# Kernel tuning notes

Measured on AMD Instinct MI355X. Metric: run time of the kernel, lower is better.

## Reference

```python
import jax, jax.numpy as jnp
import numpy as np

N, M, D, H, T = 8192, 8192, 64, 32, 8
KERNEL_SCALE = 1.0


def setup_inputs() -> dict:
    key = jax.random.key(0)
    ks = jax.random.split(key, 8)
    s1 = 1.0 / np.sqrt(D)
    s2 = 1.0 / np.sqrt(H)
    return {
        "X": jax.random.normal(ks[0], (N, D), jnp.float32),
        "Y": jax.random.normal(ks[1], (M, D), jnp.float32),
        "Y_target": jax.random.normal(ks[2], (M, T), jnp.float32),
        "W1": jax.random.normal(ks[3], (D, H), jnp.float32) * s1,
        "b1": jnp.zeros((H,), jnp.float32),
        "W2": jax.random.normal(ks[4], (H, H), jnp.float32) * s2,
        "b2": jnp.zeros((H,), jnp.float32),
        "W3": jax.random.normal(ks[5], (H, H), jnp.float32) * s2,
        "b3": jnp.zeros((H,), jnp.float32),
    }


def _mlp(x, W1, b1, W2, b2, W3, b3):
    h = jax.nn.relu(x @ W1 + b1)
    h = jax.nn.relu(h @ W2 + b2)
    return jax.nn.relu(h @ W3 + b3)


def reference(X, Y, Y_target, W1, b1, W2, b2, W3, b3):
    Xf = _mlp(X, W1, b1, W2, b2, W3, b3)  # [N, H]
    Yf = _mlp(Y, W1, b1, W2, b2, W3, b3)  # [M, H]
    sq = (
        jnp.sum(Xf * Xf, axis=1, keepdims=True)
        + jnp.sum(Yf * Yf, axis=1)[None, :]
        - 2.0 * (Xf @ Yf.T)
    )
    sq = jnp.maximum(sq, 0.0)  # guard tiny negatives from cancellation
    kernel = jnp.exp(-sq / (2.0 * KERNEL_SCALE**2))  # [N, M]
    weights = kernel / jnp.sum(kernel, axis=1, keepdims=True)
    return weights @ Y_target  # [N, T]
```

## Files before the change

kernel.cpp:

```cpp
#include <hip/hip_runtime.h>
#include <hip/hip_bf16.h>
#include <cstddef>

#define N_ROWS 8192
#define M_ROWS 8192
#define D_IN   64
#define H_DIM  32
#define T_OUT  8

#define NSPLIT   16
#define JSLICE   (M_ROWS / NSPLIT)
#define JTILE    32
#define NTILES   (JSLICE / JTILE)
#define NSTAGES  (NTILES / 2)
#define LOG2E    1.4426950408889634f
#define NHALF_SC (-0.72134752044448169f)

#define YI_OFF  8192
#define CK_OFF  16384
#define STAGEBUF 16640

typedef _Float16 half8  __attribute__((ext_vector_type(8)));
typedef _Float16 half4v __attribute__((ext_vector_type(4)));
typedef __fp16   fp16x2 __attribute__((ext_vector_type(2)));
typedef float    f32x16 __attribute__((ext_vector_type(16)));

__device__ __forceinline__ half8 ld_h8(const _Float16* p) {
    return *(const half8*)p;
}


__global__ __launch_bounds__(256) void prep_kernel(
    const float* __restrict__ X, const float* __restrict__ Y,
    const float* __restrict__ Yt,
    const float* __restrict__ W1, const float* __restrict__ b1,
    const float* __restrict__ W2, const float* __restrict__ b2,
    const float* __restrict__ W3, const float* __restrict__ b3,
    _Float16* __restrict__ fh, _Float16* __restrict__ fl,
    _Float16* __restrict__ yfi, float* __restrict__ ns)
{
    __shared__ float xs [32 * 65];
    __shared__ float w1l[64 * 36];
    __shared__ float w2l[32 * 36];
    __shared__ float w3l[32 * 36];
    __shared__ float h1t[32 * 33];
    __shared__ float h2t[32 * 33];
    __shared__ float psums[8 * 32];
    __shared__ float bl[96];

    const int tid = threadIdx.x;

    if (blockIdx.x >= 512) {
        const int idx = (blockIdx.x - 512) * 256 + tid;
        const int lane = idx & 63;
        const int jtg  = idx >> 6;
        const int g    = jtg & 3;
        const int jt   = jtg >> 2;
        const int t    = lane & 31;
        const int h    = lane >> 5;
        const int j    = jt * 32 + g * 8 + h * 4;
        union { _Float16 hh[8]; uint4 u; } V;
        #pragma unroll
        for (int i = 0; i < 4; ++i) {
            float v = (t < T_OUT) ? Yt[(size_t)(j + i) * T_OUT + t]
                                  : (t == 8 ? 1.0f : 0.0f);
            _Float16 hi = (_Float16)v;
            V.hh[i]     = hi;
            V.hh[4 + i] = (_Float16)(v - (float)hi);
        }
        *(uint4*)(yfi + (size_t)idx * 8) = V.u;
        return;
    }

    const int rowbase = blockIdx.x * 32;
    const bool isX = rowbase < N_ROWS;
    const float* src = isX ? (X + (size_t)rowbase * D_IN)
                           : (Y + (size_t)(rowbase - N_ROWS) * D_IN);

    {
        const float4* g4 = (const float4*)src;
        int i0 = tid * 2;
        float4 v0 = g4[i0], v1 = g4[i0 + 1];
        int f0 = tid * 8;
        int r = f0 >> 6, c = f0 & 63;
        float* dst = xs + r * 65 + c;
        dst[0] = v0.x; dst[1] = v0.y; dst[2] = v0.z; dst[3] = v0.w;
        dst[4] = v1.x; dst[5] = v1.y; dst[6] = v1.z; dst[7] = v1.w;
    }
    {
        const float4* g4 = (const float4*)W1;
        int i0 = tid * 2;
        float4 v0 = g4[i0], v1 = g4[i0 + 1];
        int f0 = tid * 8;
        int r = f0 >> 5, c = f0 & 31;
        float* dst = w1l + r * 36 + c;
        ((float4*)dst)[0] = v0; ((float4*)dst)[1] = v1;
    }
    {
        int f0 = tid * 4;
        int r = f0 >> 5, c = f0 & 31;
        *(float4*)(w2l + r * 36 + c) = ((const float4*)W2)[tid];
        *(float4*)(w3l + r * 36 + c) = ((const float4*)W3)[tid];
    }
    if (tid < 32) { bl[tid] = b1[tid]; bl[32 + tid] = b2[tid]; bl[64 + tid] = b3[tid]; }
    __syncthreads();

    const int r  = tid & 31;
    const int c0 = (tid >> 5) * 4;

    float4 a1 = *(const float4*)(bl + c0);
    #pragma unroll
    for (int k = 0; k < 64; ++k) {
        float xv = xs[r * 65 + k];
        float4 w = *(const float4*)(w1l + k * 36 + c0);
        a1.x = fmaf(xv, w.x, a1.x);
        a1.y = fmaf(xv, w.y, a1.y);
        a1.z = fmaf(xv, w.z, a1.z);
        a1.w = fmaf(xv, w.w, a1.w);
    }
    h1t[(c0 + 0) * 33 + r] = fmaxf(a1.x, 0.f);
    h1t[(c0 + 1) * 33 + r] = fmaxf(a1.y, 0.f);
    h1t[(c0 + 2) * 33 + r] = fmaxf(a1.z, 0.f);
    h1t[(c0 + 3) * 33 + r] = fmaxf(a1.w, 0.f);
    __syncthreads();

    float4 a2 = *(const float4*)(bl + 32 + c0);
    #pragma unroll
    for (int k = 0; k < 32; ++k) {
        float xv = h1t[k * 33 + r];
        float4 w = *(const float4*)(w2l + k * 36 + c0);
        a2.x = fmaf(xv, w.x, a2.x);
        a2.y = fmaf(xv, w.y, a2.y);
        a2.z = fmaf(xv, w.z, a2.z);
        a2.w = fmaf(xv, w.w, a2.w);
    }
    h2t[(c0 + 0) * 33 + r] = fmaxf(a2.x, 0.f);
    h2t[(c0 + 1) * 33 + r] = fmaxf(a2.y, 0.f);
    h2t[(c0 + 2) * 33 + r] = fmaxf(a2.z, 0.f);
    h2t[(c0 + 3) * 33 + r] = fmaxf(a2.w, 0.f);
    __syncthreads();

    float4 a3 = *(const float4*)(bl + 64 + c0);
    #pragma unroll
    for (int k = 0; k < 32; ++k) {
        float xv = h2t[k * 33 + r];
        float4 w = *(const float4*)(w3l + k * 36 + c0);
        a3.x = fmaf(xv, w.x, a3.x);
        a3.y = fmaf(xv, w.y, a3.y);
        a3.z = fmaf(xv, w.z, a3.z);
        a3.w = fmaf(xv, w.w, a3.w);
    }
    float v0 = fmaxf(a3.x, 0.f), v1 = fmaxf(a3.y, 0.f);
    float v2 = fmaxf(a3.z, 0.f), v3 = fmaxf(a3.w, 0.f);

    psums[(tid >> 5) * 32 + r] = v0 * v0 + v1 * v1 + v2 * v2 + v3 * v3;

    const float scale = isX ? LOG2E : 1.0f;
    union { _Float16 h[4]; uint2 u; } hh, ll;
    float sv0 = v0 * scale, sv1 = v1 * scale, sv2 = v2 * scale, sv3 = v3 * scale;
    hh.h[0] = (_Float16)sv0; hh.h[1] = (_Float16)sv1;
    hh.h[2] = (_Float16)sv2; hh.h[3] = (_Float16)sv3;
    ll.h[0] = (_Float16)(sv0 - (float)hh.h[0]);
    ll.h[1] = (_Float16)(sv1 - (float)hh.h[1]);
    ll.h[2] = (_Float16)(sv2 - (float)hh.h[2]);
    ll.h[3] = (_Float16)(sv3 - (float)hh.h[3]);
    {
        const int tile = blockIdx.x;
        const int ch = c0 >> 4, hb = (c0 >> 3) & 1, off = c0 & 7;
        const size_t fi = (((size_t)(tile * 2 + ch) * 64) + hb * 32 + r) * 8 + off;
        *(uint2*)(fh + fi) = hh.u;
        *(uint2*)(fl + fi) = ll.u;
    }

    __syncthreads();
    if (tid < 32) {
        float nrm = 0.f;
        #pragma unroll
        for (int g = 0; g < 8; ++g) nrm += psums[g * 32 + tid];
        ns[rowbase + tid] = NHALF_SC * nrm;
    }
}

__global__ __launch_bounds__(256, 4) void pair_kernel(
    const _Float16* __restrict__ fh, const _Float16* __restrict__ fl,
    const _Float16* __restrict__ yfi, const float* __restrict__ ns,
    float* __restrict__ pout, float* __restrict__ psum)
{
    __shared__ char smem[2 * STAGEBUF];

    const int tid  = threadIdx.x;
    const int wave = tid >> 6;
    const int lane = tid & 63;
    const int n    = lane & 31;
    const int h    = lane >> 5;

    const int rowtile = blockIdx.x * 4 + wave;
    const int rowbase = rowtile * 32;
    const int s       = blockIdx.y;
    const int ktile0  = (N_ROWS / 32) + s * NTILES;
    const int jstart  = s * JSLICE;

    const size_t qoff = (size_t)rowtile * 1024 + (size_t)lane * 8;
    half8 qh0 = ld_h8(fh + qoff);
    half8 qh1 = ld_h8(fh + qoff + 512);
    half8 ql0 = ld_h8(fl + qoff);
    half8 ql1 = ld_h8(fl + qoff + 512);

    const float qvn = ns[rowbase + n];

    auto prefetch = [&](int st, char* buf) {
        const int kt = ktile0 + 2 * st;
        const char* fhA = (const char*)(fh + (size_t)kt * 1024);
        const char* flA = (const char*)(fl + (size_t)kt * 1024);
        const char* fhB = (const char*)(fh + (size_t)(kt + 1) * 1024);
        const char* flB = (const char*)(fl + (size_t)(kt + 1) * 1024);
        const char* yA  = (const char*)(yfi + (size_t)(s * NTILES + 2 * st) * 2048);
        const char* yB  = (const char*)(yfi + (size_t)(s * NTILES + 2 * st + 1) * 2048);
        #pragma unroll
        for (int r = 0; r < 4; ++r) {
            const int c0 = wave * 64 + r * 256;
            const int c  = c0 + lane;
            const char* g; char* l;
            if (c0 < 128)      { g = fhA + (size_t)c * 16;         l = buf + c * 16; }
            else if (c0 < 256) { g = flA + (size_t)(c - 128) * 16; l = buf + 2048 + (c - 128) * 16; }
            else if (c0 < 384) { g = fhB + (size_t)(c - 256) * 16; l = buf + 4096 + (c - 256) * 16; }
            else if (c0 < 512) { g = flB + (size_t)(c - 384) * 16; l = buf + 6144 + (c - 384) * 16; }
            else if (c0 < 768) { g = yA  + (size_t)(c - 512) * 16; l = buf + YI_OFF + (c - 512) * 16; }
            else               { g = yB  + (size_t)(c - 768) * 16; l = buf + YI_OFF + 4096 + (c - 768) * 16; }
            __builtin_amdgcn_global_load_lds(
                (const __attribute__((address_space(1))) void*)g,
                (__attribute__((address_space(3))) void*)l, 16, 0, 0);
        }
        if (wave == 0) {
            const char* gc = (const char*)(ns + N_ROWS + jstart + st * 64 + lane);
            __builtin_amdgcn_global_load_lds(
                (const __attribute__((address_space(1))) void*)gc,
                (__attribute__((address_space(3))) void*)(buf + CK_OFF), 4, 0, 0);
        }
    };

    f32x16 o = {};

    auto compute = [&](const char* buf, int sub) {
        const char* kb = buf + sub * 4096;
        half8 kh0 = *(const half8*)(kb + lane * 16);
        half8 kh1 = *(const half8*)(kb + 1024 + lane * 16);
        half8 kl0 = *(const half8*)(kb + 2048 + lane * 16);
        half8 kl1 = *(const half8*)(kb + 3072 + lane * 16);

        f32x16 acc = {};
        acc = __builtin_amdgcn_mfma_f32_32x32x16_f16(kh0, qh0, acc, 0, 0, 0);
        acc = __builtin_amdgcn_mfma_f32_32x32x16_f16(kh1, qh1, acc, 0, 0, 0);
        acc = __builtin_amdgcn_mfma_f32_32x32x16_f16(kh0, ql0, acc, 0, 0, 0);
        acc = __builtin_amdgcn_mfma_f32_32x32x16_f16(kh1, ql1, acc, 0, 0, 0);
        acc = __builtin_amdgcn_mfma_f32_32x32x16_f16(kl0, qh0, acc, 0, 0, 0);
        acc = __builtin_amdgcn_mfma_f32_32x32x16_f16(kl1, qh1, acc, 0, 0, 0);

        const char* ckb = buf + CK_OFF + sub * 128;
        const char* yb  = buf + YI_OFF + sub * 4096;
        #pragma unroll
        for (int g = 0; g < 4; ++g) {
            float4 ck4 = *(const float4*)(ckb + (8 * g + 4 * h) * 4);
            float w0 = __builtin_amdgcn_exp2f(fminf(acc[4*g+0] + (ck4.x + qvn), 0.f));
            float w1 = __builtin_amdgcn_exp2f(fminf(acc[4*g+1] + (ck4.y + qvn), 0.f));
            float w2 = __builtin_amdgcn_exp2f(fminf(acc[4*g+2] + (ck4.z + qvn), 0.f));
            float w3 = __builtin_amdgcn_exp2f(fminf(acc[4*g+3] + (ck4.w + qvn), 0.f));
            union { unsigned int u[2]; half4v v; } ph;
            ph.u[0] = __builtin_bit_cast(unsigned int, __builtin_amdgcn_cvt_pkrtz(w0, w1));
            ph.u[1] = __builtin_bit_cast(unsigned int, __builtin_amdgcn_cvt_pkrtz(w2, w3));
            uint4 yv = *(const uint4*)(yb + (g * 64 + lane) * 16);
            union { unsigned int u[2]; half4v v; } yh, yl;
            yh.u[0] = yv.x; yh.u[1] = yv.y;
            yl.u[0] = yv.z; yl.u[1] = yv.w;
            o = __builtin_amdgcn_mfma_f32_32x32x8f16(ph.v, yh.v, o, 0, 0, 0);
            o = __builtin_amdgcn_mfma_f32_32x32x8f16(ph.v, yl.v, o, 0, 0, 0);
        }
    };

    prefetch(0, smem);
    __syncthreads();

    for (int st = 0; st < NSTAGES; ++st) {
        char* cur = smem + (st & 1) * STAGEBUF;
        if (st + 1 < NSTAGES) prefetch(st + 1, smem + ((st + 1) & 1) * STAGEBUF);
        compute(cur, 0);
        compute(cur, 1);
        __syncthreads();
    }

    const int t = n;
    if (t <= 8) {
        #pragma unroll
        for (int r = 0; r < 16; ++r) {
            int i = (r & 3) + 8 * (r >> 2) + 4 * h;
            int row = rowbase + i;
            float v = o[r];
            if (t < 8)
                pout[((size_t)s * N_ROWS + row) * T_OUT + t] = v;
            else
                psum[(size_t)s * N_ROWS + row] = v;
        }
    }
}

__global__ __launch_bounds__(256) void reduce_kernel(
    const float* __restrict__ pout, const float* __restrict__ psum,
    float* __restrict__ out)
{
    const int id = blockIdx.x * 256 + threadIdx.x;
    const int i = id >> 3;
    float sv = 0.f, sw = 0.f;
    #pragma unroll
    for (int s = 0; s < NSPLIT; ++s) {
        sv += pout[(size_t)s * N_ROWS * T_OUT + id];
        sw += psum[(size_t)s * N_ROWS + i];
    }
    out[id] = sv / sw;
}

extern "C" void kernel_launch(void* const* d_in, const int* in_sizes, int n_in,
                              void* d_out, int out_size, void* d_ws, size_t ws_size,
                              hipStream_t stream)
{
    const float* X  = (const float*)d_in[0];
    const float* Y  = (const float*)d_in[1];
    const float* Yt = (const float*)d_in[2];
    const float* W1 = (const float*)d_in[3];
    const float* b1 = (const float*)d_in[4];
    const float* W2 = (const float*)d_in[5];
    const float* b2 = (const float*)d_in[6];
    const float* W3 = (const float*)d_in[7];
    const float* b3 = (const float*)d_in[8];
    float* out = (float*)d_out;

    char* ws = (char*)d_ws;
    const size_t n_feat = (size_t)((N_ROWS + M_ROWS) / 32) * 2 * 512;
    _Float16* fh  = (_Float16*)ws;   ws += n_feat * 2;
    _Float16* fl  = (_Float16*)ws;   ws += n_feat * 2;
    const size_t n_yfi = (size_t)(M_ROWS / JTILE) * 4 * 64 * 8;
    _Float16* yfi = (_Float16*)ws;   ws += n_yfi * 2;
    float*    ns  = (float*)ws;      ws += (N_ROWS + M_ROWS) * 4;
    float*    pout = (float*)ws;     ws += (size_t)NSPLIT * N_ROWS * T_OUT * 4;
    float*    psum = (float*)ws;

    prep_kernel<<<512 + 256, 256, 0, stream>>>(
        X, Y, Yt, W1, b1, W2, b2, W3, b3, fh, fl, yfi, ns);

    dim3 grid2(N_ROWS / 128, NSPLIT);
    pair_kernel<<<grid2, 256, 0, stream>>>(fh, fl, yfi, ns, pout, psum);

    reduce_kernel<<<(N_ROWS * T_OUT) / 256, 256, 0, stream>>>(pout, psum, out);
}
```

Before: 103.8 us.

## Process two query row tiles per wave to reuse staged key tiles

Each wave now handles two 32-row query tiles against every key tile loaded into LDS. This halves the LDS and global traffic per query row and gives the scheduler two independent MFMA chains to interleave. The split count over keys doubles so the grid keeps the same number of blocks, and the occupancy hint drops from 4 to 3 because each wave holds twice the accumulators and query registers. The cost is more register pressure and twice as many partial results for the reduce kernel to sum.

```diff
diff --git a/kernel.cpp b/kernel.cpp
--- a/kernel.cpp
+++ b/kernel.cpp
@@ -8,7 +8,7 @@
 #define H_DIM  32
 #define T_OUT  8
 
-#define NSPLIT   16
+#define NSPLIT   32
 #define JSLICE   (M_ROWS / NSPLIT)
 #define JTILE    32
 #define NTILES   (JSLICE / JTILE)
@@ -181,7 +181,7 @@
     }
 }
 
-__global__ __launch_bounds__(256, 4) void pair_kernel(
+__global__ __launch_bounds__(256, 3) void pair_kernel(
     const _Float16* __restrict__ fh, const _Float16* __restrict__ fl,
     const _Float16* __restrict__ yfi, const float* __restrict__ ns,
     float* __restrict__ pout, float* __restrict__ psum)
@@ -194,19 +194,26 @@
     const int n    = lane & 31;
     const int h    = lane >> 5;
 
-    const int rowtile = blockIdx.x * 4 + wave;
-    const int rowbase = rowtile * 32;
-    const int s       = blockIdx.y;
-    const int ktile0  = (N_ROWS / 32) + s * NTILES;
-    const int jstart  = s * JSLICE;
-
-    const size_t qoff = (size_t)rowtile * 1024 + (size_t)lane * 8;
-    half8 qh0 = ld_h8(fh + qoff);
-    half8 qh1 = ld_h8(fh + qoff + 512);
-    half8 ql0 = ld_h8(fl + qoff);
-    half8 ql1 = ld_h8(fl + qoff + 512);
-
-    const float qvn = ns[rowbase + n];
+    const int rt0      = blockIdx.x * 8 + wave * 2;
+    const int rowbase0 = rt0 * 32;
+    const int rowbase1 = rowbase0 + 32;
+    const int s        = blockIdx.y;
+    const int ktile0   = (N_ROWS / 32) + s * NTILES;
+    const int jstart   = s * JSLICE;
+
+    const size_t qoffA = (size_t)rt0 * 1024 + (size_t)lane * 8;
+    const size_t qoffB = qoffA + 1024;
+    half8 qAh0 = ld_h8(fh + qoffA);
+    half8 qAh1 = ld_h8(fh + qoffA + 512);
+    half8 qAl0 = ld_h8(fl + qoffA);
+    half8 qAl1 = ld_h8(fl + qoffA + 512);
+    half8 qBh0 = ld_h8(fh + qoffB);
+    half8 qBh1 = ld_h8(fh + qoffB + 512);
+    half8 qBl0 = ld_h8(fl + qoffB);
+    half8 qBl1 = ld_h8(fl + qoffB + 512);
+
+    const float qvnA = ns[rowbase0 + n];
+    const float qvnB = ns[rowbase1 + n];
 
     auto prefetch = [&](int st, char* buf) {
         const int kt = ktile0 + 2 * st;
@@ -239,7 +246,7 @@
         }
     };
 
-    f32x16 o = {};
+    f32x16 oA = {}, oB = {};
 
     auto compute = [&](const char* buf, int sub) {
         const char* kb = buf + sub * 4096;
@@ -248,32 +255,46 @@
         half8 kl0 = *(const half8*)(kb + 2048 + lane * 16);
         half8 kl1 = *(const half8*)(kb + 3072 + lane * 16);
 
-        f32x16 acc = {};
-        acc = __builtin_amdgcn_mfma_f32_32x32x16_f16(kh0, qh0, acc, 0, 0, 0);
-        acc = __builtin_amdgcn_mfma_f32_32x32x16_f16(kh1, qh1, acc, 0, 0, 0);
-        acc = __builtin_amdgcn_mfma_f32_32x32x16_f16(kh0, ql0, acc, 0, 0, 0);
-        acc = __builtin_amdgcn_mfma_f32_32x32x16_f16(kh1, ql1, acc, 0, 0, 0);
-        acc = __builtin_amdgcn_mfma_f32_32x32x16_f16(kl0, qh0, acc, 0, 0, 0);
-        acc = __builtin_amdgcn_mfma_f32_32x32x16_f16(kl1, qh1, acc, 0, 0, 0);
+        f32x16 accA = {}, accB = {};
+        accA = __builtin_amdgcn_mfma_f32_32x32x16_f16(kh0, qAh0, accA, 0, 0, 0);
+        accB = __builtin_amdgcn_mfma_f32_32x32x16_f16(kh0, qBh0, accB, 0, 0, 0);
+        accA = __builtin_amdgcn_mfma_f32_32x32x16_f16(kh1, qAh1, accA, 0, 0, 0);
+        accB = __builtin_amdgcn_mfma_f32_32x32x16_f16(kh1, qBh1, accB, 0, 0, 0);
+        accA = __builtin_amdgcn_mfma_f32_32x32x16_f16(kh0, qAl0, accA, 0, 0, 0);
+        accB = __builtin_amdgcn_mfma_f32_32x32x16_f16(kh0, qBl0, accB, 0, 0, 0);
+        accA = __builtin_amdgcn_mfma_f32_32x32x16_f16(kh1, qAl1, accA, 0, 0, 0);
+        accB = __builtin_amdgcn_mfma_f32_32x32x16_f16(kh1, qBl1, accB, 0, 0, 0);
+        accA = __builtin_amdgcn_mfma_f32_32x32x16_f16(kl0, qAh0, accA, 0, 0, 0);
+        accB = __builtin_amdgcn_mfma_f32_32x32x16_f16(kl0, qBh0, accB, 0, 0, 0);
+        accA = __builtin_amdgcn_mfma_f32_32x32x16_f16(kl1, qAh1, accA, 0, 0, 0);
+        accB = __builtin_amdgcn_mfma_f32_32x32x16_f16(kl1, qBh1, accB, 0, 0, 0);
 
         const char* ckb = buf + CK_OFF + sub * 128;
         const char* yb  = buf + YI_OFF + sub * 4096;
         #pragma unroll
         for (int g = 0; g < 4; ++g) {
             float4 ck4 = *(const float4*)(ckb + (8 * g + 4 * h) * 4);
-            float w0 = __builtin_amdgcn_exp2f(fminf(acc[4*g+0] + (ck4.x + qvn), 0.f));
-            float w1 = __builtin_amdgcn_exp2f(fminf(acc[4*g+1] + (ck4.y + qvn), 0.f));
-            float w2 = __builtin_amdgcn_exp2f(fminf(acc[4*g+2] + (ck4.z + qvn), 0.f));
-            float w3 = __builtin_amdgcn_exp2f(fminf(acc[4*g+3] + (ck4.w + qvn), 0.f));
-            union { unsigned int u[2]; half4v v; } ph;
-            ph.u[0] = __builtin_bit_cast(unsigned int, __builtin_amdgcn_cvt_pkrtz(w0, w1));
-            ph.u[1] = __builtin_bit_cast(unsigned int, __builtin_amdgcn_cvt_pkrtz(w2, w3));
+            float a0 = __builtin_amdgcn_exp2f(fminf(accA[4*g+0] + (ck4.x + qvnA), 0.f));
+            float a1 = __builtin_amdgcn_exp2f(fminf(accA[4*g+1] + (ck4.y + qvnA), 0.f));
+            float a2 = __builtin_amdgcn_exp2f(fminf(accA[4*g+2] + (ck4.z + qvnA), 0.f));
+            float a3 = __builtin_amdgcn_exp2f(fminf(accA[4*g+3] + (ck4.w + qvnA), 0.f));
+            float b0 = __builtin_amdgcn_exp2f(fminf(accB[4*g+0] + (ck4.x + qvnB), 0.f));
+            float b1 = __builtin_amdgcn_exp2f(fminf(accB[4*g+1] + (ck4.y + qvnB), 0.f));
+            float b2 = __builtin_amdgcn_exp2f(fminf(accB[4*g+2] + (ck4.z + qvnB), 0.f));
+            float b3 = __builtin_amdgcn_exp2f(fminf(accB[4*g+3] + (ck4.w + qvnB), 0.f));
+            union { unsigned int u[2]; half4v v; } pA, pB;
+            pA.u[0] = __builtin_bit_cast(unsigned int, __builtin_amdgcn_cvt_pkrtz(a0, a1));
+            pA.u[1] = __builtin_bit_cast(unsigned int, __builtin_amdgcn_cvt_pkrtz(a2, a3));
+            pB.u[0] = __builtin_bit_cast(unsigned int, __builtin_amdgcn_cvt_pkrtz(b0, b1));
+            pB.u[1] = __builtin_bit_cast(unsigned int, __builtin_amdgcn_cvt_pkrtz(b2, b3));
             uint4 yv = *(const uint4*)(yb + (g * 64 + lane) * 16);
             union { unsigned int u[2]; half4v v; } yh, yl;
             yh.u[0] = yv.x; yh.u[1] = yv.y;
             yl.u[0] = yv.z; yl.u[1] = yv.w;
-            o = __builtin_amdgcn_mfma_f32_32x32x8f16(ph.v, yh.v, o, 0, 0, 0);
-            o = __builtin_amdgcn_mfma_f32_32x32x8f16(ph.v, yl.v, o, 0, 0, 0);
+            oA = __builtin_amdgcn_mfma_f32_32x32x8f16(pA.v, yh.v, oA, 0, 0, 0);
+            oB = __builtin_amdgcn_mfma_f32_32x32x8f16(pB.v, yh.v, oB, 0, 0, 0);
+            oA = __builtin_amdgcn_mfma_f32_32x32x8f16(pA.v, yl.v, oA, 0, 0, 0);
+            oB = __builtin_amdgcn_mfma_f32_32x32x8f16(pB.v, yl.v, oB, 0, 0, 0);
         }
     };
 
@@ -293,12 +314,14 @@
         #pragma unroll
         for (int r = 0; r < 16; ++r) {
             int i = (r & 3) + 8 * (r >> 2) + 4 * h;
-            int row = rowbase + i;
-            float v = o[r];
-            if (t < 8)
-                pout[((size_t)s * N_ROWS + row) * T_OUT + t] = v;
-            else
-                psum[(size_t)s * N_ROWS + row] = v;
+            float vA = oA[r], vB = oB[r];
+            if (t < 8) {
+                pout[((size_t)s * N_ROWS + rowbase0 + i) * T_OUT + t] = vA;
+                pout[((size_t)s * N_ROWS + rowbase1 + i) * T_OUT + t] = vB;
+            } else {
+                psum[(size_t)s * N_ROWS + rowbase0 + i] = vA;
+                psum[(size_t)s * N_ROWS + rowbase1 + i] = vB;
+            }
         }
     }
 }
@@ -346,7 +369,7 @@
     prep_kernel<<<512 + 256, 256, 0, stream>>>(
         X, Y, Yt, W1, b1, W2, b2, W3, b3, fh, fl, yfi, ns);
 
-    dim3 grid2(N_ROWS / 128, NSPLIT);
+    dim3 grid2(N_ROWS / 256, NSPLIT);
     pair_kernel<<<grid2, 256, 0, stream>>>(fh, fl, yfi, ns, pout, psum);
 
     reduce_kernel<<<(N_ROWS * T_OUT) / 256, 256, 0, stream>>>(pout, psum, out);
```

New measurement: 107.2 us. +3.3%, slower.
